# Kernel optimization log

Measured on AMD Instinct MI355X. Metric: run time of the kernel, lower is better.

## Reference

```python
import jax, jax.numpy as jnp
import numpy as np

B, S, D_IN, D_OUT = 4, 4096, 768, 64


def setup_inputs() -> dict:
    key = jax.random.key(0)
    kx, kq, kk, kv = jax.random.split(key, 4)
    x = jax.random.normal(kx, (B, S, D_IN), dtype=jnp.float32)
    # kaiming-uniform-ish scale for weights
    bound = 1.0 / np.sqrt(D_IN)
    Wq = jax.random.uniform(kq, (D_IN, D_OUT), jnp.float32, -bound, bound)
    Wk = jax.random.uniform(kk, (D_IN, D_OUT), jnp.float32, -bound, bound)
    Wv = jax.random.uniform(kv, (D_IN, D_OUT), jnp.float32, -bound, bound)
    return {"x": x, "Wq": Wq, "Wk": Wk, "Wv": Wv}


def reference(x, Wq, Wk, Wv):
    # QKV projections (qkv_bias=False)
    q = jnp.einsum("bsi,io->bso", x, Wq)  # [B,S,D_OUT]
    k = jnp.einsum("bsi,io->bso", x, Wk)
    v = jnp.einsum("bsi,io->bso", x, Wv)
    # scores [B,S,S], causal mask (upper triangle excl. diag -> -inf)
    scores = jnp.einsum("bqd,bkd->bqk", q, k)
    num_tokens = x.shape[1]
    causal = jnp.triu(jnp.ones((num_tokens, num_tokens), dtype=bool), k=1)
    scores = jnp.where(causal[None, :, :], -jnp.inf, scores)
    scale = 1.0 / np.sqrt(k.shape[-1]).astype(np.float32)
    attn = jax.nn.softmax(scores * scale, axis=-1)
    # dropout: eval mode -> identity (module's custom Dropout is a no-op when not training)
    ctx = jnp.einsum("bqk,bkv->bqv", attn, v)  # [B,S,D_OUT]
    return ctx
```

## Files before the change

kernel.cpp:

```cpp
#include <hip/hip_runtime.h>
#include <stdint.h>

#define KSTEPS 24
#define TOKENS 16384

typedef short short8 __attribute__((ext_vector_type(8)));
typedef float fx4 __attribute__((ext_vector_type(4)));
typedef unsigned short u16;
typedef u16 u16x4 __attribute__((ext_vector_type(4)));

static __device__ __forceinline__ u16 f2bf(float f) {
  union { float f; unsigned u; } v; v.f = f;
  return (u16)((v.u + 0x7fffu + ((v.u >> 16) & 1u)) >> 16);
}

static __device__ __forceinline__ u16 p2bf(float f) {
  union { float f; unsigned u; } v; v.f = f;
  return (u16)((v.u + 0x8000u) >> 16);
}

static __device__ __forceinline__ fx4 mfma16(short8 a, short8 b, fx4 c) {
  return __builtin_amdgcn_mfma_f32_16x16x32_bf16(a, b, c, 0, 0, 0);
}

static __device__ __forceinline__ void async16(const void* g, void* l) {
  __builtin_amdgcn_global_load_lds(
      (const __attribute__((address_space(1))) void*)g,
      (__attribute__((address_space(3))) void*)(unsigned int)(uintptr_t)l,
      16, 0, 0);
}

__global__ void prep_w_kernel(const float* __restrict__ Wq, const float* __restrict__ Wk,
                              const float* __restrict__ Wv, u16* __restrict__ wfrag) {
  int idx  = blockIdx.x * 256 + threadIdx.x;
  int lane = idx & 63;
  int fid  = idx >> 6;
  int nt   = fid & 3;
  int ks   = (fid >> 2) % KSTEPS;
  int mat  = fid / (KSTEPS * 4);
  const float* W = (mat == 0) ? Wq : (mat == 1) ? Wk : Wv;
  int n  = nt * 16 + (lane & 15);
  int k0 = ks * 32 + (lane >> 4) * 8;
  short8 out;
#pragma unroll
  for (int j = 0; j < 8; j++) out[j] = (short)f2bf(W[(size_t)(k0 + j) * 64 + n]);
  *(short8*)(wfrag + (size_t)idx * 8) = out;
}

__global__ __launch_bounds__(256) void proj_kernel(const float* __restrict__ x,
                                                   const u16* __restrict__ wfrag,
                                                   u16* __restrict__ qb,
                                                   u16* __restrict__ kb,
                                                   u16* __restrict__ vT) {
  __shared__ float xs[2][32 * 32];
  __shared__ u16  Ws[2][12 * 512];

  int w = threadIdx.x >> 6, lane = threadIdx.x & 63;
  int ln = lane & 15, quad = lane >> 4;
  int rw = w >> 1, cs = w & 1;
  int s0 = blockIdx.x * 32;

  fx4 acc[6];
#pragma unroll
  for (int j = 0; j < 6; j++) acc[j] = (fx4){0.f, 0.f, 0.f, 0.f};

  int srow  = w * 8 + (lane >> 3);
  int slot  = lane & 7;
  int chunk = slot ^ (srow & 7);
  const float* xsrc = x + (size_t)(s0 + srow) * 768 + chunk * 4;

#pragma unroll
  for (int m = 0; m < 3; m++)
    async16(wfrag + ((size_t)(m * KSTEPS + 0) * 256 + w * 64 + lane) * 8,
            (char*)Ws[0] + m * 4096 + w * 1024 + lane * 16);
  async16(xsrc, (char*)xs[0] + w * 1024 + lane * 16);

  int r = rw * 16 + ln;
  for (int ks = 0; ks < KSTEPS; ks++) {
    __syncthreads();
    if (ks < KSTEPS - 1) {
      int buf = (ks + 1) & 1;
#pragma unroll
      for (int m = 0; m < 3; m++)
        async16(wfrag + ((size_t)(m * KSTEPS + ks + 1) * 256 + w * 64 + lane) * 8,
                (char*)Ws[buf] + m * 4096 + w * 1024 + lane * 16);
      async16(xsrc + (ks + 1) * 32, (char*)xs[buf] + w * 1024 + lane * 16);
    }
    const float* xb = xs[ks & 1];
    const u16*  wb = Ws[ks & 1];
    int sl0 = (2 * quad)     ^ (r & 7);
    int sl1 = (2 * quad + 1) ^ (r & 7);
    fx4 xa = *(const fx4*)(xb + r * 32 + sl0 * 4);
    fx4 xv = *(const fx4*)(xb + r * 32 + sl1 * 4);
    short8 af;
#pragma unroll
    for (int j = 0; j < 4; j++) { af[j] = (short)f2bf(xa[j]); af[4 + j] = (short)f2bf(xv[j]); }
#pragma unroll
    for (int j = 0; j < 6; j++) {
      short8 bf = *(const short8*)(wb + (cs * 6 + j) * 512 + lane * 8);
      acc[j] = mfma16(af, bf, acc[j]);
    }
  }

  int tok0 = s0 + rw * 16 + quad * 4;
#pragma unroll
  for (int j = 0; j < 6; j++) {
    int f = cs * 6 + j;
    int d = (f & 3) * 16 + ln;
    if (f < 4) {
#pragma unroll
      for (int reg = 0; reg < 4; reg++)
        qb[(size_t)(tok0 + reg) * 64 + d] = f2bf(acc[j][reg] * 0.180336887f);
    } else if (f < 8) {
#pragma unroll
      for (int reg = 0; reg < 4; reg++)
        kb[(size_t)(tok0 + reg) * 64 + d] = f2bf(acc[j][reg]);
    } else {
      int b = tok0 >> 12, s = tok0 & 4095;
      u16x4 vp;
#pragma unroll
      for (int reg = 0; reg < 4; reg++) vp[reg] = f2bf(acc[j][reg]);
      *(u16x4*)(vT + ((size_t)b * 64 + d) * 4096 + s) = vp;
    }
  }
}

__global__ __launch_bounds__(256, 3) void attn_kernel(const u16* __restrict__ qb,
                                                      const u16* __restrict__ kb,
                                                      const u16* __restrict__ vT,
                                                      float* __restrict__ o0g,
                                                      float* __restrict__ po5,
                                                      float* __restrict__ mlb) {
  __shared__ u16 Kstg[2][4096];
  __shared__ u16 Vstg[2][4096];
  __shared__ u16 Ps[4][32 * 72];

  int w = threadIdx.x >> 6, lane = threadIdx.x & 63;
  int ln = lane & 15, quad = lane >> 4;
  int band = 31 - blockIdx.x;
  int b = blockIdx.y, z = blockIdx.z;
  int q0 = band * 128;
  int qw = q0 + w * 32;

  const u16* qbb = qb + (size_t)b * 4096 * 64;
  const u16* kbb = kb + (size_t)b * 4096 * 64;
  const u16* vtb = vT + (size_t)b * 64 * 4096;

  short8 qf0a = *(const short8*)(qbb + (size_t)(qw + ln) * 64 + quad * 8);
  short8 qf1a = *(const short8*)(qbb + (size_t)(qw + ln) * 64 + 32 + quad * 8);
  short8 qf0b = *(const short8*)(qbb + (size_t)(qw + 16 + ln) * 64 + quad * 8);
  short8 qf1b = *(const short8*)(qbb + (size_t)(qw + 16 + ln) * 64 + 32 + quad * 8);

  short8 ones;
#pragma unroll
  for (int j = 0; j < 8; j++) ones[j] = (short)0x3F80;

  fx4 oa[4], ob[4];
#pragma unroll
  for (int j = 0; j < 4; j++) { oa[j] = (fx4){0.f,0.f,0.f,0.f}; ob[j] = (fx4){0.f,0.f,0.f,0.f}; }
  float la[4] = {0.f,0.f,0.f,0.f}, lb[4] = {0.f,0.f,0.f,0.f};

  int n = 2 * band + 2;
  int c = (n + 5) / 6;
  int lo = z * c; if (lo > n) lo = n;
  int hi = lo + c; if (hi > n) hi = n;

  int t0c = w * 64 + lane;
  if (lo < hi) {
#pragma unroll
    for (int j = 0; j < 2; j++) {
      int cc = t0c + j * 256;
      int row = cc >> 3, slot = cc & 7, sw_ = (slot ^ (row & 7)) * 8;
      async16(kbb + ((size_t)lo * 64 + row) * 64 + sw_, (char*)Kstg[0] + cc * 16);
      async16(vtb + (size_t)row * 4096 + lo * 64 + sw_, (char*)Vstg[0] + cc * 16);
    }
  }

  for (int t = lo; t < hi; t++) {
    __syncthreads();
    if (t + 1 < hi) {
      int nb = (t - lo + 1) & 1;
#pragma unroll
      for (int j = 0; j < 2; j++) {
        int cc = t0c + j * 256;
        int row = cc >> 3, slot = cc & 7, sw_ = (slot ^ (row & 7)) * 8;
        async16(kbb + ((size_t)(t + 1) * 64 + row) * 64 + sw_, (char*)Kstg[nb] + cc * 16);
        async16(vtb + (size_t)row * 4096 + (t + 1) * 64 + sw_, (char*)Vstg[nb] + cc * 16);
      }
    }
    if (64 * t > qw + 31) continue;

    const u16* Kb = Kstg[(t - lo) & 1];
    const u16* Vb = Vstg[(t - lo) & 1];

    fx4 sAa[4], sAb[4];
#pragma unroll
    for (int nt = 0; nt < 4; nt++) {
      int row = nt * 16 + ln;
      int s0_ = quad ^ (row & 7), s1_ = (quad + 4) ^ (row & 7);
      short8 kf0 = *(const short8*)(Kb + (row * 8 + s0_) * 8);
      short8 kf1 = *(const short8*)(Kb + (row * 8 + s1_) * 8);
      sAa[nt] = mfma16(qf0a, kf0, (fx4){0.f,0.f,0.f,0.f});
      sAa[nt] = mfma16(qf1a, kf1, sAa[nt]);
      sAb[nt] = mfma16(qf0b, kf0, (fx4){0.f,0.f,0.f,0.f});
      sAb[nt] = mfma16(qf1b, kf1, sAb[nt]);
    }

    if (64 * t + 63 > qw) {
#pragma unroll
      for (int nt = 0; nt < 4; nt++)
#pragma unroll
        for (int reg = 0; reg < 4; reg++) {
          int col = t * 64 + nt * 16 + ln;
          int ra = qw + quad * 4 + reg;
          if (col > ra) sAa[nt][reg] = -1e30f;
          if (col > ra + 16) sAb[nt][reg] = -1e30f;
        }
    }

#pragma unroll
    for (int nt = 0; nt < 4; nt++)
#pragma unroll
      for (int reg = 0; reg < 4; reg++) {
        Ps[w][(quad * 4 + reg) * 72 + nt * 16 + ln] =
            p2bf(__builtin_amdgcn_exp2f(sAa[nt][reg]));
        Ps[w][(16 + quad * 4 + reg) * 72 + nt * 16 + ln] =
            p2bf(__builtin_amdgcn_exp2f(sAb[nt][reg]));
      }

    short8 pf0a = *(const short8*)(&Ps[w][ln * 72 + quad * 8]);
    short8 pf1a = *(const short8*)(&Ps[w][ln * 72 + 32 + quad * 8]);
    short8 pf0b = *(const short8*)(&Ps[w][(16 + ln) * 72 + quad * 8]);
    short8 pf1b = *(const short8*)(&Ps[w][(16 + ln) * 72 + 32 + quad * 8]);

    fx4 lacc = mfma16(pf0a, ones, (fx4){0.f,0.f,0.f,0.f});
    lacc = mfma16(pf1a, ones, lacc);
#pragma unroll
    for (int reg = 0; reg < 4; reg++) la[reg] += lacc[reg];
    lacc = mfma16(pf0b, ones, (fx4){0.f,0.f,0.f,0.f});
    lacc = mfma16(pf1b, ones, lacc);
#pragma unroll
    for (int reg = 0; reg < 4; reg++) lb[reg] += lacc[reg];

#pragma unroll
    for (int nt2 = 0; nt2 < 4; nt2++) {
      int row = nt2 * 16 + ln;
      int s0_ = quad ^ (row & 7), s1_ = (quad + 4) ^ (row & 7);
      short8 vf0 = *(const short8*)(Vb + (row * 8 + s0_) * 8);
      short8 vf1 = *(const short8*)(Vb + (row * 8 + s1_) * 8);
      oa[nt2] = mfma16(pf0a, vf0, oa[nt2]);
      oa[nt2] = mfma16(pf1a, vf1, oa[nt2]);
      ob[nt2] = mfma16(pf0b, vf0, ob[nt2]);
      ob[nt2] = mfma16(pf1b, vf1, ob[nt2]);
    }
  }

  float* dst = (z == 0) ? o0g : (po5 + (size_t)(z - 1) * 4 * 4096 * 64);
#pragma unroll
  for (int nt2 = 0; nt2 < 4; nt2++)
#pragma unroll
    for (int reg = 0; reg < 4; reg++) {
      int ra = qw + quad * 4 + reg;
      dst[((size_t)b * 4096 + ra) * 64 + nt2 * 16 + ln] = oa[nt2][reg];
      dst[((size_t)b * 4096 + ra + 16) * 64 + nt2 * 16 + ln] = ob[nt2][reg];
    }
  if (ln == 0) {
#pragma unroll
    for (int reg = 0; reg < 4; reg++) {
      int ra = qw + quad * 4 + reg;
      mlb[((size_t)z * 4 + b) * 4096 + ra] = la[reg];
      mlb[((size_t)z * 4 + b) * 4096 + ra + 16] = lb[reg];
    }
  }
}

__global__ __launch_bounds__(256) void merge_kernel(float* __restrict__ out,
                                                    const float* __restrict__ po5,
                                                    const float* __restrict__ mlb) {
  int qt = blockIdx.x, b = blockIdx.y;
  int r = threadIdx.x >> 3;
  int c = (threadIdx.x & 7) * 8;
  size_t row = (size_t)b * 4096 + qt * 32 + r;
  float l = mlb[row];
#pragma unroll
  for (int z = 1; z < 6; z++) l += mlb[(size_t)z * 4 * 4096 + row];
  float inv = 1.0f / l;
  float* op = out + row * 64 + c;
  fx4 u0 = *(fx4*)op, u1 = *(fx4*)(op + 4);
#pragma unroll
  for (int z = 1; z < 6; z++) {
    const float* pp = po5 + (size_t)(z - 1) * 4 * 4096 * 64 + row * 64 + c;
    fx4 v0 = *(const fx4*)pp, v1 = *(const fx4*)(pp + 4);
#pragma unroll
    for (int j = 0; j < 4; j++) { u0[j] += v0[j]; u1[j] += v1[j]; }
  }
#pragma unroll
  for (int j = 0; j < 4; j++) { u0[j] *= inv; u1[j] *= inv; }
  *(fx4*)op = u0;
  *(fx4*)(op + 4) = u1;
}

extern "C" void kernel_launch(void* const* d_in, const int* in_sizes, int n_in,
                              void* d_out, int out_size, void* d_ws, size_t ws_size,
                              hipStream_t stream) {
  const float* x  = (const float*)d_in[0];
  const float* Wq = (const float*)d_in[1];
  const float* Wk = (const float*)d_in[2];
  const float* Wv = (const float*)d_in[3];

  u16* qbw = (u16*)d_ws;
  u16* kbw = qbw + (size_t)TOKENS * 64;
  u16* vtw = kbw + (size_t)TOKENS * 64;
  u16* wfr = vtw + (size_t)TOKENS * 64;
  float* po5 = (float*)(wfr + (size_t)3 * KSTEPS * 256 * 8);
  float* mlb = po5 + (size_t)5 * 4 * 4096 * 64;

  prep_w_kernel<<<72, 256, 0, stream>>>(Wq, Wk, Wv, wfr);
  proj_kernel<<<TOKENS / 32, 256, 0, stream>>>(x, wfr, qbw, kbw, vtw);
  attn_kernel<<<dim3(32, 4, 6), 256, 0, stream>>>(qbw, kbw, vtw,
                                                  (float*)d_out, po5, mlb);
  merge_kernel<<<dim3(128, 4), 256, 0, stream>>>((float*)d_out, po5, mlb);
}
```

Baseline: 136.6 us.

## Keep weight fragments in registers and stream x directly in projection kernel

The projection kernel is restructured to use 768-thread blocks with 12 waves. Each wave owns one 16-column output tile of Q, K or V and holds all 24 weight k-step fragments in registers. It then loops over four 16-token row tiles, reading x straight from global memory with a two-step register prefetch, and drops the LDS double-buffering and barriers entirely. The aim is to remove shared-memory staging and sync overhead, but each x row is now loaded from global memory by 12 waves, and the 24 short8 weight registers raise register pressure.

```diff
diff --git a/kernel.cpp b/kernel.cpp
--- a/kernel.cpp
+++ b/kernel.cpp
@@ -47,79 +47,65 @@
   *(short8*)(wfrag + (size_t)idx * 8) = out;
 }
 
-__global__ __launch_bounds__(256) void proj_kernel(const float* __restrict__ x,
-                                                   const u16* __restrict__ wfrag,
-                                                   u16* __restrict__ qb,
-                                                   u16* __restrict__ kb,
-                                                   u16* __restrict__ vT) {
-  __shared__ float xs[2][32 * 32];
-  __shared__ u16  Ws[2][12 * 512];
-
+__global__ __launch_bounds__(768, 3) void proj_kernel(const float* __restrict__ x,
+                                                      const u16* __restrict__ wfrag,
+                                                      u16* __restrict__ qb,
+                                                      u16* __restrict__ kb,
+                                                      u16* __restrict__ vT) {
   int w = threadIdx.x >> 6, lane = threadIdx.x & 63;
   int ln = lane & 15, quad = lane >> 4;
-  int rw = w >> 1, cs = w & 1;
-  int s0 = blockIdx.x * 32;
-
-  fx4 acc[6];
-#pragma unroll
-  for (int j = 0; j < 6; j++) acc[j] = (fx4){0.f, 0.f, 0.f, 0.f};
-
-  int srow  = w * 8 + (lane >> 3);
-  int slot  = lane & 7;
-  int chunk = slot ^ (srow & 7);
-  const float* xsrc = x + (size_t)(s0 + srow) * 768 + chunk * 4;
-
-#pragma unroll
-  for (int m = 0; m < 3; m++)
-    async16(wfrag + ((size_t)(m * KSTEPS + 0) * 256 + w * 64 + lane) * 8,
-            (char*)Ws[0] + m * 4096 + w * 1024 + lane * 16);
-  async16(xsrc, (char*)xs[0] + w * 1024 + lane * 16);
-
-  int r = rw * 16 + ln;
-  for (int ks = 0; ks < KSTEPS; ks++) {
-    __syncthreads();
-    if (ks < KSTEPS - 1) {
-      int buf = (ks + 1) & 1;
-#pragma unroll
-      for (int m = 0; m < 3; m++)
-        async16(wfrag + ((size_t)(m * KSTEPS + ks + 1) * 256 + w * 64 + lane) * 8,
-                (char*)Ws[buf] + m * 4096 + w * 1024 + lane * 16);
-      async16(xsrc + (ks + 1) * 32, (char*)xs[buf] + w * 1024 + lane * 16);
-    }
-    const float* xb = xs[ks & 1];
-    const u16*  wb = Ws[ks & 1];
-    int sl0 = (2 * quad)     ^ (r & 7);
-    int sl1 = (2 * quad + 1) ^ (r & 7);
-    fx4 xa = *(const fx4*)(xb + r * 32 + sl0 * 4);
-    fx4 xv = *(const fx4*)(xb + r * 32 + sl1 * 4);
-    short8 af;
-#pragma unroll
-    for (int j = 0; j < 4; j++) { af[j] = (short)f2bf(xa[j]); af[4 + j] = (short)f2bf(xv[j]); }
-#pragma unroll
-    for (int j = 0; j < 6; j++) {
-      short8 bf = *(const short8*)(wb + (cs * 6 + j) * 512 + lane * 8);
-      acc[j] = mfma16(af, bf, acc[j]);
-    }
-  }
-
-  int tok0 = s0 + rw * 16 + quad * 4;
-#pragma unroll
-  for (int j = 0; j < 6; j++) {
-    int f = cs * 6 + j;
-    int d = (f & 3) * 16 + ln;
-    if (f < 4) {
+  int m = w >> 2, nt = w & 3;
+
+  short8 wreg[KSTEPS];
+  const u16* wp = wfrag + ((size_t)m * KSTEPS * 256 + nt * 64 + lane) * 8;
+#pragma unroll
+  for (int ks = 0; ks < KSTEPS; ks++)
+    wreg[ks] = *(const short8*)(wp + (size_t)ks * 2048);
+
+  for (int i = 0; i < 4; i++) {
+    int s0 = (blockIdx.x * 4 + i) * 16;
+    const float* xp = x + (size_t)(s0 + ln) * 768 + quad * 8;
+
+    fx4 acc = (fx4){0.f, 0.f, 0.f, 0.f};
+    fx4 xr[2][2];
+#pragma unroll
+    for (int s = 0; s < 2; s++) {
+      xr[s][0] = *(const fx4*)(xp + s * 32);
+      xr[s][1] = *(const fx4*)(xp + s * 32 + 4);
+    }
+#pragma unroll 4
+    for (int ks = 0; ks < KSTEPS; ks++) {
+      int c = ks & 1;
+      short8 af;
+#pragma unroll
+      for (int j = 0; j < 4; j++) {
+        af[j]     = (short)f2bf(xr[c][0][j]);
+        af[4 + j] = (short)f2bf(xr[c][1][j]);
+      }
+      fx4 nx0, nx1;
+      if (ks < KSTEPS - 2) {
+        nx0 = *(const fx4*)(xp + (ks + 2) * 32);
+        nx1 = *(const fx4*)(xp + (ks + 2) * 32 + 4);
+      }
+      acc = mfma16(af, wreg[ks], acc);
+      if (ks < KSTEPS - 2) { xr[c][0] = nx0; xr[c][1] = nx1; }
+    }
+
+    int tok0 = s0 + quad * 4;
+    int d = nt * 16 + ln;
+    if (m == 0) {
 #pragma unroll
       for (int reg = 0; reg < 4; reg++)
-        qb[(size_t)(tok0 + reg) * 64 + d] = f2bf(acc[j][reg] * 0.180336887f);
-    } else if (f < 8) {
+        qb[(size_t)(tok0 + reg) * 64 + d] = f2bf(acc[reg] * 0.180336887f);
+    } else if (m == 1) {
 #pragma unroll
       for (int reg = 0; reg < 4; reg++)
-        kb[(size_t)(tok0 + reg) * 64 + d] = f2bf(acc[j][reg]);
+        kb[(size_t)(tok0 + reg) * 64 + d] = f2bf(acc[reg]);
     } else {
       int b = tok0 >> 12, s = tok0 & 4095;
       u16x4 vp;
 #pragma unroll
-      for (int reg = 0; reg < 4; reg++) vp[reg] = f2bf(acc[j][reg]);
+      for (int reg = 0; reg < 4; reg++) vp[reg] = f2bf(acc[reg]);
       *(u16x4*)(vT + ((size_t)b * 64 + d) * 4096 + s) = vp;
     }
   }
@@ -316,7 +302,7 @@
   float* mlb = po5 + (size_t)5 * 4 * 4096 * 64;
 
   prep_w_kernel<<<72, 256, 0, stream>>>(Wq, Wk, Wv, wfr);
-  proj_kernel<<<TOKENS / 32, 256, 0, stream>>>(x, wfr, qbw, kbw, vtw);
+  proj_kernel<<<TOKENS / 64, 768, 0, stream>>>(x, wfr, qbw, kbw, vtw);
   attn_kernel<<<dim3(32, 4, 6), 256, 0, stream>>>(qbw, kbw, vtw,
                                                   (float*)d_out, po5, mlb);
   merge_kernel<<<dim3(128, 4), 256, 0, stream>>>((float*)d_out, po5, mlb);
```

Result: slower. 238.1 us (+74.3%).

## Widen projection tiles to 64 tokens and store split-K partials as bf16

Applied to the files above, without the earlier changes.

The projection kernel now handles 64 tokens per block with two row tiles per wave, so each weight fragment staged in shared memory is reused twice and half as many blocks reload the weights. The attention kernel writes all six key-split partial outputs as bf16 into a workspace instead of fp32, with split 0 no longer going straight to the output. The merge kernel sums all six bf16 partials and normalises. This halves partial-output traffic but adds bf16 rounding to the unnormalised partial sums.

```diff
diff --git a/kernel.cpp b/kernel.cpp
--- a/kernel.cpp
+++ b/kernel.cpp
@@ -8,6 +8,7 @@
 typedef float fx4 __attribute__((ext_vector_type(4)));
 typedef unsigned short u16;
 typedef u16 u16x4 __attribute__((ext_vector_type(4)));
+typedef u16 u16x8 __attribute__((ext_vector_type(8)));
 
 static __device__ __forceinline__ u16 f2bf(float f) {
   union { float f; unsigned u; } v; v.f = f;
@@ -17,6 +18,11 @@
 static __device__ __forceinline__ u16 p2bf(float f) {
   union { float f; unsigned u; } v; v.f = f;
   return (u16)((v.u + 0x8000u) >> 16);
+}
+
+static __device__ __forceinline__ float bf2f(u16 h) {
+  union { unsigned u; float f; } v; v.u = ((unsigned)h) << 16;
+  return v.f;
 }
 
 static __device__ __forceinline__ fx4 mfma16(short8 a, short8 b, fx4 c) {
@@ -52,75 +58,96 @@
                                                    u16* __restrict__ qb,
                                                    u16* __restrict__ kb,
                                                    u16* __restrict__ vT) {
-  __shared__ float xs[2][32 * 32];
+  __shared__ float xs[2][64 * 32];
   __shared__ u16  Ws[2][12 * 512];
 
   int w = threadIdx.x >> 6, lane = threadIdx.x & 63;
   int ln = lane & 15, quad = lane >> 4;
   int rw = w >> 1, cs = w & 1;
-  int s0 = blockIdx.x * 32;
-
-  fx4 acc[6];
-#pragma unroll
-  for (int j = 0; j < 6; j++) acc[j] = (fx4){0.f, 0.f, 0.f, 0.f};
-
-  int srow  = w * 8 + (lane >> 3);
-  int slot  = lane & 7;
-  int chunk = slot ^ (srow & 7);
-  const float* xsrc = x + (size_t)(s0 + srow) * 768 + chunk * 4;
-
-#pragma unroll
-  for (int m = 0; m < 3; m++)
-    async16(wfrag + ((size_t)(m * KSTEPS + 0) * 256 + w * 64 + lane) * 8,
-            (char*)Ws[0] + m * 4096 + w * 1024 + lane * 16);
-  async16(xsrc, (char*)xs[0] + w * 1024 + lane * 16);
-
-  int r = rw * 16 + ln;
+  int s0 = blockIdx.x * 64;
+
+  fx4 acc[2][6];
+#pragma unroll
+  for (int rt = 0; rt < 2; rt++)
+#pragma unroll
+    for (int j = 0; j < 6; j++) acc[rt][j] = (fx4){0.f, 0.f, 0.f, 0.f};
+
+#define STAGE_X(ks, buf)                                                       \
+  {                                                                            \
+    _Pragma("unroll")                                                          \
+    for (int j = 0; j < 2; j++) {                                              \
+      int cc = (w * 2 + j) * 64 + lane;                                        \
+      int row = cc >> 3, c = cc & 7, sc = c ^ (row & 7);                       \
+      async16(x + (size_t)(s0 + row) * 768 + (ks) * 32 + sc * 4,               \
+              (char*)xs[buf] + cc * 16);                                       \
+    }                                                                          \
+  }
+#define STAGE_W(ks, buf)                                                       \
+  {                                                                            \
+    _Pragma("unroll")                                                          \
+    for (int m = 0; m < 3; m++)                                                \
+      async16(wfrag + ((size_t)(m * KSTEPS + (ks)) * 256 + w * 64 + lane) * 8, \
+              (char*)Ws[buf] + (m * 4 + w) * 1024 + lane * 16);                \
+  }
+
+  STAGE_X(0, 0);
+  STAGE_W(0, 0);
+
   for (int ks = 0; ks < KSTEPS; ks++) {
     __syncthreads();
     if (ks < KSTEPS - 1) {
-      int buf = (ks + 1) & 1;
-#pragma unroll
-      for (int m = 0; m < 3; m++)
-        async16(wfrag + ((size_t)(m * KSTEPS + ks + 1) * 256 + w * 64 + lane) * 8,
-                (char*)Ws[buf] + m * 4096 + w * 1024 + lane * 16);
-      async16(xsrc + (ks + 1) * 32, (char*)xs[buf] + w * 1024 + lane * 16);
+      int nb = (ks + 1) & 1;
+      STAGE_X(ks + 1, nb);
+      STAGE_W(ks + 1, nb);
     }
     const float* xb = xs[ks & 1];
     const u16*  wb = Ws[ks & 1];
-    int sl0 = (2 * quad)     ^ (r & 7);
-    int sl1 = (2 * quad + 1) ^ (r & 7);
-    fx4 xa = *(const fx4*)(xb + r * 32 + sl0 * 4);
-    fx4 xv = *(const fx4*)(xb + r * 32 + sl1 * 4);
-    short8 af;
-#pragma unroll
-    for (int j = 0; j < 4; j++) { af[j] = (short)f2bf(xa[j]); af[4 + j] = (short)f2bf(xv[j]); }
+    short8 af[2];
+#pragma unroll
+    for (int rt = 0; rt < 2; rt++) {
+      int r = rw * 32 + rt * 16 + ln;
+      int sl0 = (2 * quad) ^ (r & 7);
+      int sl1 = (2 * quad + 1) ^ (r & 7);
+      fx4 xa = *(const fx4*)(xb + r * 32 + sl0 * 4);
+      fx4 xv = *(const fx4*)(xb + r * 32 + sl1 * 4);
+#pragma unroll
+      for (int j = 0; j < 4; j++) {
+        af[rt][j] = (short)f2bf(xa[j]);
+        af[rt][4 + j] = (short)f2bf(xv[j]);
+      }
+    }
 #pragma unroll
     for (int j = 0; j < 6; j++) {
       short8 bf = *(const short8*)(wb + (cs * 6 + j) * 512 + lane * 8);
-      acc[j] = mfma16(af, bf, acc[j]);
-    }
-  }
-
-  int tok0 = s0 + rw * 16 + quad * 4;
-#pragma unroll
-  for (int j = 0; j < 6; j++) {
-    int f = cs * 6 + j;
-    int d = (f & 3) * 16 + ln;
-    if (f < 4) {
-#pragma unroll
-      for (int reg = 0; reg < 4; reg++)
-        qb[(size_t)(tok0 + reg) * 64 + d] = f2bf(acc[j][reg] * 0.180336887f);
-    } else if (f < 8) {
-#pragma unroll
-      for (int reg = 0; reg < 4; reg++)
-        kb[(size_t)(tok0 + reg) * 64 + d] = f2bf(acc[j][reg]);
-    } else {
-      int b = tok0 >> 12, s = tok0 & 4095;
-      u16x4 vp;
-#pragma unroll
-      for (int reg = 0; reg < 4; reg++) vp[reg] = f2bf(acc[j][reg]);
-      *(u16x4*)(vT + ((size_t)b * 64 + d) * 4096 + s) = vp;
+      acc[0][j] = mfma16(af[0], bf, acc[0][j]);
+      acc[1][j] = mfma16(af[1], bf, acc[1][j]);
+    }
+  }
+#undef STAGE_X
+#undef STAGE_W
+
+#pragma unroll
+  for (int rt = 0; rt < 2; rt++) {
+    int tok0 = s0 + rw * 32 + rt * 16 + quad * 4;
+#pragma unroll
+    for (int j = 0; j < 6; j++) {
+      int f = cs * 6 + j;
+      int d = (f & 3) * 16 + ln;
+      if (f < 4) {
+#pragma unroll
+        for (int reg = 0; reg < 4; reg++)
+          qb[(size_t)(tok0 + reg) * 64 + d] = f2bf(acc[rt][j][reg] * 0.180336887f);
+      } else if (f < 8) {
+#pragma unroll
+        for (int reg = 0; reg < 4; reg++)
+          kb[(size_t)(tok0 + reg) * 64 + d] = f2bf(acc[rt][j][reg]);
+      } else {
+        int b = tok0 >> 12, s = tok0 & 4095;
+        u16x4 vp;
+#pragma unroll
+        for (int reg = 0; reg < 4; reg++) vp[reg] = f2bf(acc[rt][j][reg]);
+        *(u16x4*)(vT + ((size_t)b * 64 + d) * 4096 + s) = vp;
+      }
     }
   }
 }
@@ -128,8 +155,7 @@
 __global__ __launch_bounds__(256, 3) void attn_kernel(const u16* __restrict__ qb,
                                                       const u16* __restrict__ kb,
                                                       const u16* __restrict__ vT,
-                                                      float* __restrict__ o0g,
-                                                      float* __restrict__ po5,
+                                                      u16* __restrict__ pob,
                                                       float* __restrict__ mlb) {
   __shared__ u16 Kstg[2][4096];
   __shared__ u16 Vstg[2][4096];
@@ -255,14 +281,14 @@
     }
   }
 
-  float* dst = (z == 0) ? o0g : (po5 + (size_t)(z - 1) * 4 * 4096 * 64);
+  u16* dst = pob + (size_t)z * (4 * 4096 * 64);
 #pragma unroll
   for (int nt2 = 0; nt2 < 4; nt2++)
 #pragma unroll
     for (int reg = 0; reg < 4; reg++) {
       int ra = qw + quad * 4 + reg;
-      dst[((size_t)b * 4096 + ra) * 64 + nt2 * 16 + ln] = oa[nt2][reg];
-      dst[((size_t)b * 4096 + ra + 16) * 64 + nt2 * 16 + ln] = ob[nt2][reg];
+      dst[((size_t)b * 4096 + ra) * 64 + nt2 * 16 + ln] = p2bf(oa[nt2][reg]);
+      dst[((size_t)b * 4096 + ra + 16) * 64 + nt2 * 16 + ln] = p2bf(ob[nt2][reg]);
     }
   if (ln == 0) {
 #pragma unroll
@@ -275,29 +301,29 @@
 }
 
 __global__ __launch_bounds__(256) void merge_kernel(float* __restrict__ out,
-                                                    const float* __restrict__ po5,
+                                                    const u16* __restrict__ pob,
                                                     const float* __restrict__ mlb) {
   int qt = blockIdx.x, b = blockIdx.y;
   int r = threadIdx.x >> 3;
   int c = (threadIdx.x & 7) * 8;
   size_t row = (size_t)b * 4096 + qt * 32 + r;
-  float l = mlb[row];
-#pragma unroll
-  for (int z = 1; z < 6; z++) l += mlb[(size_t)z * 4 * 4096 + row];
+  float l = 0.f;
+#pragma unroll
+  for (int z = 0; z < 6; z++) l += mlb[(size_t)z * 4 * 4096 + row];
   float inv = 1.0f / l;
+  float acc[8];
+#pragma unroll
+  for (int j = 0; j < 8; j++) acc[j] = 0.f;
+#pragma unroll
+  for (int z = 0; z < 6; z++) {
+    const u16* pp = pob + (size_t)z * (4 * 4096 * 64) + row * 64 + c;
+    u16x8 v = *(const u16x8*)pp;
+#pragma unroll
+    for (int j = 0; j < 8; j++) acc[j] += bf2f(v[j]);
+  }
   float* op = out + row * 64 + c;
-  fx4 u0 = *(fx4*)op, u1 = *(fx4*)(op + 4);
-#pragma unroll
-  for (int z = 1; z < 6; z++) {
-    const float* pp = po5 + (size_t)(z - 1) * 4 * 4096 * 64 + row * 64 + c;
-    fx4 v0 = *(const fx4*)pp, v1 = *(const fx4*)(pp + 4);
-#pragma unroll
-    for (int j = 0; j < 4; j++) { u0[j] += v0[j]; u1[j] += v1[j]; }
-  }
-#pragma unroll
-  for (int j = 0; j < 4; j++) { u0[j] *= inv; u1[j] *= inv; }
-  *(fx4*)op = u0;
-  *(fx4*)(op + 4) = u1;
+#pragma unroll
+  for (int j = 0; j < 8; j++) op[j] = acc[j] * inv;
 }
 
 extern "C" void kernel_launch(void* const* d_in, const int* in_sizes, int n_in,
@@ -312,12 +338,11 @@
   u16* kbw = qbw + (size_t)TOKENS * 64;
   u16* vtw = kbw + (size_t)TOKENS * 64;
   u16* wfr = vtw + (size_t)TOKENS * 64;
-  float* po5 = (float*)(wfr + (size_t)3 * KSTEPS * 256 * 8);
-  float* mlb = po5 + (size_t)5 * 4 * 4096 * 64;
+  u16* pob = wfr + (size_t)3 * KSTEPS * 256 * 8;
+  float* mlb = (float*)(pob + (size_t)6 * 4 * 4096 * 64);
 
   prep_w_kernel<<<72, 256, 0, stream>>>(Wq, Wk, Wv, wfr);
-  proj_kernel<<<TOKENS / 32, 256, 0, stream>>>(x, wfr, qbw, kbw, vtw);
-  attn_kernel<<<dim3(32, 4, 6), 256, 0, stream>>>(qbw, kbw, vtw,
-                                                  (float*)d_out, po5, mlb);
-  merge_kernel<<<dim3(128, 4), 256, 0, stream>>>((float*)d_out, po5, mlb);
-}
+  proj_kernel<<<TOKENS / 64, 256, 0, stream>>>(x, wfr, qbw, kbw, vtw);
+  attn_kernel<<<dim3(32, 4, 6), 256, 0, stream>>>(qbw, kbw, vtw, pob, mlb);
+  merge_kernel<<<dim3(128, 4), 256, 0, stream>>>((float*)d_out, pob, mlb);
+}
```

Result: faster. 133.7 us (-2.1%).
